# Kernel optimization log

Measured on AMD Instinct MI355X. Metric: run time of the kernel, lower is better.

## Reference

```python
import jax, jax.numpy as jnp
import numpy as np

D_MODEL = 512
D_FF = 2048
D_STATE = 16
D_CONV = 4
EXPAND = 2
D_INNER = EXPAND * D_MODEL
DT_RANK = (D_MODEL + 15) // 16  # 32
EPS = 1e-5


def silu(x):
    return x * jax.nn.sigmoid(x)


def layernorm(x, g, b):
    mu = jnp.mean(x, axis=-1, keepdims=True)
    var = jnp.mean(jnp.square(x - mu), axis=-1, keepdims=True)
    return (x - mu) * jax.lax.rsqrt(var + EPS) * g + b


def mamba_block(x, in_w, conv_w, conv_b, xproj_w, dt_w, dt_b, A_log, Dp, out_w):
    # x: (B, L, d_model)
    Bsz, L, _ = x.shape
    di = conv_w.shape[0]
    k = conv_w.shape[1]
    n = A_log.shape[1]
    r = dt_w.shape[1]
    xz = x @ in_w.T                      # (B, L, 2*di)
    xi, z = jnp.split(xz, 2, axis=-1)
    # causal depthwise conv1d
    xt = jnp.transpose(xi, (0, 2, 1))    # (B, di, L)
    xt = jnp.pad(xt, ((0, 0), (0, 0), (k - 1, 0)))
    xc = jax.lax.conv_general_dilated(
        xt, conv_w[:, None, :], (1,), 'VALID',
        feature_group_count=di,
        dimension_numbers=('NCH', 'OIH', 'NCH'))
    xc = silu(xc + conv_b[None, :, None])
    xc = jnp.transpose(xc, (0, 2, 1))    # (B, L, di)
    dbc = xc @ xproj_w.T                 # (B, L, r + 2n)
    dt = jax.nn.softplus(dbc[..., :r] @ dt_w.T + dt_b)   # (B, L, di)
    Bm = dbc[..., r:r + n]               # (B, L, n)
    Cm = dbc[..., r + n:]                # (B, L, n)
    A = -jnp.exp(A_log)                  # (di, n)

    def step(h, inp):
        dt_t, B_t, C_t, x_t = inp        # (B,di), (B,n), (B,n), (B,di)
        dA = jnp.exp(dt_t[..., None] * A)                 # (B, di, n)
        h = dA * h + (dt_t * x_t)[..., None] * B_t[:, None, :]
        y = jnp.einsum('bdn,bn->bd', h, C_t)
        return h, y

    xs = (jnp.moveaxis(dt, 1, 0), jnp.moveaxis(Bm, 1, 0),
          jnp.moveaxis(Cm, 1, 0), jnp.moveaxis(xc, 1, 0))
    h0 = jnp.zeros((Bsz, di, n), x.dtype)
    _, ys = jax.lax.scan(step, h0, xs)
    y = jnp.moveaxis(ys, 0, 1) + xc * Dp  # (B, L, di)
    y = y * silu(z)
    return y @ out_w.T                    # (B, L, d_model)


def setup_inputs() -> dict:
    key = jax.random.key(0)
    ks = iter(jax.random.split(key, 40))
    s = 0.02

    def mamba_params():
        return dict(
            in_w=jax.random.normal(next(ks), (2 * D_INNER, D_MODEL), jnp.float32) * s,
            conv_w=jax.random.normal(next(ks), (D_INNER, D_CONV), jnp.float32) * 0.3,
            conv_b=jnp.zeros((D_INNER,), jnp.float32),
            xproj_w=jax.random.normal(next(ks), (DT_RANK + 2 * D_STATE, D_INNER), jnp.float32) * s,
            dt_w=jax.random.normal(next(ks), (D_INNER, DT_RANK), jnp.float32) * 0.1,
            dt_b=jax.random.uniform(next(ks), (D_INNER,), jnp.float32, -4.0, -2.0),
            A_log=jnp.tile(jnp.log(jnp.arange(1, D_STATE + 1, dtype=jnp.float32)), (D_INNER, 1)),
            D=jnp.ones((D_INNER,), jnp.float32),
            out_w=jax.random.normal(next(ks), (D_MODEL, D_INNER), jnp.float32) * s,
        )

    pf = mamba_params()
    pb = mamba_params()
    inp = dict(
        x=jax.random.normal(next(ks), (8, 4096, D_MODEL), jnp.float32),
        f_in_w=pf['in_w'], f_conv_w=pf['conv_w'], f_conv_b=pf['conv_b'],
        f_xproj_w=pf['xproj_w'], f_dt_w=pf['dt_w'], f_dt_b=pf['dt_b'],
        f_A_log=pf['A_log'], f_D=pf['D'], f_out_w=pf['out_w'],
        b_in_w=pb['in_w'], b_conv_w=pb['conv_w'], b_conv_b=pb['conv_b'],
        b_xproj_w=pb['xproj_w'], b_dt_w=pb['dt_w'], b_dt_b=pb['dt_b'],
        b_A_log=pb['A_log'], b_D=pb['D'], b_out_w=pb['out_w'],
        ln_f_g=jnp.ones((D_MODEL,), jnp.float32), ln_f_b=jnp.zeros((D_MODEL,), jnp.float32),
        ln_b_g=jnp.ones((D_MODEL,), jnp.float32), ln_b_b=jnp.zeros((D_MODEL,), jnp.float32),
        ln_ff_g=jnp.ones((D_MODEL,), jnp.float32), ln_ff_b=jnp.zeros((D_MODEL,), jnp.float32),
        ffn_w1=jax.random.normal(next(ks), (D_FF, D_MODEL), jnp.float32) * s,
        ffn_b1=jnp.zeros((D_FF,), jnp.float32),
        ffn_w2=jax.random.normal(next(ks), (D_MODEL, D_FF), jnp.float32) * s,
        ffn_b2=jnp.zeros((D_MODEL,), jnp.float32),
    )
    return inp


def reference(x,
              f_in_w, f_conv_w, f_conv_b, f_xproj_w, f_dt_w, f_dt_b, f_A_log, f_D, f_out_w,
              b_in_w, b_conv_w, b_conv_b, b_xproj_w, b_dt_w, b_dt_b, b_A_log, b_D, b_out_w,
              ln_f_g, ln_f_b, ln_b_g, ln_b_b, ln_ff_g, ln_ff_b,
              ffn_w1, ffn_b1, ffn_w2, ffn_b2):
    # forward-direction mamba + AddNorm (dropout is identity at eval)
    mf = mamba_block(x, f_in_w, f_conv_w, f_conv_b, f_xproj_w, f_dt_w, f_dt_b,
                     f_A_log, f_D, f_out_w)
    out_f = layernorm(x + mf, ln_f_g, ln_f_b)
    # backward-direction: flip along seq, mamba, flip back
    mb = mamba_block(jnp.flip(x, axis=1), b_in_w, b_conv_w, b_conv_b, b_xproj_w,
                     b_dt_w, b_dt_b, b_A_log, b_D, b_out_w)
    out_b = jnp.flip(mb, axis=1)
    h = 0.5 * (out_f + layernorm(x + out_b, ln_b_g, ln_b_b))
    # FFN + AddNorm
    ff = jax.nn.gelu(h @ ffn_w1.T + ffn_b1) @ ffn_w2.T + ffn_b2
    return layernorm(h + ff, ln_ff_g, ln_ff_b)
```

## Files before the change

### kernel.cpp

```cpp
#include <hip/hip_runtime.h>
#include <hip/hip_bf16.h>
#include <math.h>


#define LSEQ 4096
#define DIN 1024
#define NST 16
#define CHUNK 64
#define NCHUNK 64
#define TCH 16

typedef __attribute__((ext_vector_type(8))) short bf16x8;
typedef __attribute__((ext_vector_type(4))) float f32x4;

typedef const __attribute__((address_space(1))) void* gas_ptr;
typedef __attribute__((address_space(3))) void* las_ptr;

__device__ __forceinline__ void load_lds16(const void* g, void* l) {
  __builtin_amdgcn_global_load_lds((gas_ptr)g, (las_ptr)l, 16, 0, 0);
}

__device__ __forceinline__ unsigned short bf16bits(float v) {
  __hip_bfloat16 h = __float2bfloat16(v);
  return *reinterpret_cast<unsigned short*>(&h);
}

__global__ void cast_bf16x4_kernel(const float4* __restrict__ src,
                                   ushort4* __restrict__ dst, int n4) {
  int i = blockIdx.x * 256 + threadIdx.x;
  if (i < n4) {
    float4 v = src[i];
    ushort4 o = {bf16bits(v.x), bf16bits(v.y), bf16bits(v.z), bf16bits(v.w)};
    dst[i] = o;
  }
}

__global__ void pad_xproj_kernel(const float* __restrict__ src,
                                 __hip_bfloat16* __restrict__ dst) {
  int i = blockIdx.x * 256 + threadIdx.x;
  int r = i >> 10, c = i & 1023;
  float v = (r < 64) ? src[r * 1024 + c] : 0.f;
  dst[i] = __float2bfloat16(v);
}

__global__ void zero4_kernel(float4* __restrict__ p, int n4) {
  int i = blockIdx.x * 256 + threadIdx.x;
  if (i < n4) p[i] = (float4){0.f, 0.f, 0.f, 0.f};
}

enum { EPI_BF16 = 0, EPI_F32 = 1, EPI_GELU_BF16 = 2, EPI_BIAS_BF16 = 3,
       EPI_F32_ATOM = 4, EPI_SPLIT_BF16 = 5 };

template <int EPI, int KSPLIT = 1>
__launch_bounds__(256)
__global__ void gemm_bt(const __hip_bfloat16* __restrict__ A,
                        const __hip_bfloat16* __restrict__ W,
                        void* __restrict__ Cout,
                        const float* __restrict__ bias,
                        void* __restrict__ Cout2,
                        int M, int N, int K) {
  __shared__ __align__(16) __hip_bfloat16 sA[128 * 64];
  __shared__ __align__(16) __hip_bfloat16 sB[128 * 64];
  const int tid  = threadIdx.x;
  const int wave = tid >> 6;
  const int lane = tid & 63;
  const int tileM = blockIdx.y * 128;
  const int tileN = blockIdx.x * 128;
  const int wrow = (wave >> 1) * 64;
  const int wcol = (wave & 1) * 64;

  f32x4 acc[4][4];
#pragma unroll
  for (int i = 0; i < 4; i++)
#pragma unroll
    for (int j = 0; j < 4; j++) acc[i][j] = (f32x4){0.f, 0.f, 0.f, 0.f};

  const int rbase = wave * 8 + (lane >> 3);
  const int segel = (((lane & 7) ^ (lane >> 3)) << 3);
  const int fr = lane & 15;
  const int fq = lane >> 4;

  const int kspan = K / KSPLIT;
  const int kbeg = (KSPLIT > 1) ? (int)blockIdx.z * kspan : 0;

  for (int k0 = kbeg; k0 < kbeg + kspan; k0 += 64) {
#pragma unroll
    for (int i = 0; i < 4; i++) {
      int r = i * 32 + rbase;
      const __hip_bfloat16* ga = A + (size_t)(tileM + r) * K + k0 + segel;
      const __hip_bfloat16* gb = W + (size_t)(tileN + r) * K + k0 + segel;
      int ldsoff = (i * 32 + wave * 8) * 64;
      load_lds16(ga, (void*)&sA[ldsoff]);
      load_lds16(gb, (void*)&sB[ldsoff]);
    }
    __syncthreads();
#pragma unroll
    for (int kt = 0; kt < 2; kt++) {
      bf16x8 af[4], bfm[4];
#pragma unroll
      for (int mt = 0; mt < 4; mt++) {
        int rm = wrow + mt * 16 + fr;
        int sg = (kt * 4 + fq) ^ (rm & 7);
        af[mt] = *(const bf16x8*)&sA[rm * 64 + sg * 8];
      }
#pragma unroll
      for (int nt = 0; nt < 4; nt++) {
        int rn = wcol + nt * 16 + fr;
        int sg = (kt * 4 + fq) ^ (rn & 7);
        bfm[nt] = *(const bf16x8*)&sB[rn * 64 + sg * 8];
      }
#pragma unroll
      for (int mt = 0; mt < 4; mt++)
#pragma unroll
        for (int nt = 0; nt < 4; nt++)
          acc[mt][nt] = __builtin_amdgcn_mfma_f32_16x16x32_bf16(
              af[mt], bfm[nt], acc[mt][nt], 0, 0, 0);
    }
    __syncthreads();
  }

#pragma unroll
  for (int mt = 0; mt < 4; mt++) {
#pragma unroll
    for (int nt = 0; nt < 4; nt++) {
      int col = tileN + wcol + nt * 16 + fr;
#pragma unroll
      for (int i = 0; i < 4; i++) {
        int row = tileM + wrow + mt * 16 + fq * 4 + i;
        float v = acc[mt][nt][i];
        size_t off = (size_t)row * N + col;
        if constexpr (EPI == EPI_BF16) {
          ((__hip_bfloat16*)Cout)[off] = __float2bfloat16(v);
        } else if constexpr (EPI == EPI_F32) {
          ((float*)Cout)[off] = v;
        } else if constexpr (EPI == EPI_F32_ATOM) {
          atomicAdd((float*)Cout + off, v);
        } else if constexpr (EPI == EPI_GELU_BF16) {
          float t = v + bias[col];
          float u0 = t + 0.044715f * t * t * t;
          float g = __fdividef(t, 1.f + __expf(-1.5957691216057308f * u0));
          ((__hip_bfloat16*)Cout)[off] = __float2bfloat16(g);
        } else if constexpr (EPI == EPI_BIAS_BF16) {
          ((__hip_bfloat16*)Cout)[off] = __float2bfloat16(v + bias[col]);
        } else {
          __hip_bfloat16* dst =
              (tileN < 1024) ? (__hip_bfloat16*)Cout : (__hip_bfloat16*)Cout2;
          int c2 = (tileN < 1024) ? col : (col - 1024);
          dst[(size_t)row * 1024 + c2] = __float2bfloat16(v);
        }
      }
    }
  }
}

__global__ void conv_silu_kernel(const __hip_bfloat16* __restrict__ xi,
                                 const float* __restrict__ cw,
                                 const float* __restrict__ cb,
                                 __hip_bfloat16* __restrict__ xc, int dir) {
  int row0 = blockIdx.x * TCH;
  int b = row0 >> 12, t0 = row0 & 4095;
  int d0 = threadIdx.x << 2;
  float w[4][4];
#pragma unroll
  for (int u = 0; u < 4; u++) {
    float4 wv = ((const float4*)cw)[d0 + u];
    w[u][0] = wv.x; w[u][1] = wv.y; w[u][2] = wv.z; w[u][3] = wv.w;
  }
  float4 bv = *(const float4*)(cb + d0);

  float win[3][4];
  auto loadrow = [&](int tau, float* o) {
    if (tau < 0) {
      o[0] = o[1] = o[2] = o[3] = 0.f;
    } else {
      int l = dir ? (LSEQ - 1 - tau) : tau;
      ushort4 v = *(const ushort4*)(xi + ((size_t)(b * LSEQ + l)) * DIN + d0);
      o[0] = __uint_as_float((unsigned)v.x << 16);
      o[1] = __uint_as_float((unsigned)v.y << 16);
      o[2] = __uint_as_float((unsigned)v.z << 16);
      o[3] = __uint_as_float((unsigned)v.w << 16);
    }
  };
  loadrow(t0 - 3, win[0]);
  loadrow(t0 - 2, win[1]);
  loadrow(t0 - 1, win[2]);

#pragma unroll
  for (int i = 0; i < TCH; i++) {
    int t = t0 + i;
    float cur[4];
    loadrow(t, cur);
    unsigned short o[4];
#pragma unroll
    for (int u = 0; u < 4; u++) {
      float s = (u == 0) ? bv.x : (u == 1) ? bv.y : (u == 2) ? bv.z : bv.w;
      s += w[u][0] * win[0][u] + w[u][1] * win[1][u] + w[u][2] * win[2][u] +
           w[u][3] * cur[u];
      float val = __fdividef(s, 1.f + __expf(-s));
      o[u] = bf16bits(val);
    }
    ushort4 o4 = {o[0], o[1], o[2], o[3]};
    *(ushort4*)(xc + (size_t)(row0 + i) * DIN + d0) = o4;
#pragma unroll
    for (int u = 0; u < 4; u++) {
      win[0][u] = win[1][u]; win[1][u] = win[2][u]; win[2][u] = cur[u];
    }
  }
}

__global__ void scan_pass1(const __hip_bfloat16* __restrict__ xc,
                           const float* __restrict__ dbc,
                           const float* __restrict__ dtw,
                           const float* __restrict__ dtbias,
                           __hip_bfloat16* __restrict__ dtb,
                           float* __restrict__ sumdt, float* __restrict__ hend) {
  __shared__ __align__(16) float sdbc[64 * 64];
  int d = blockIdx.x * 256 + threadIdx.x;
  int c = blockIdx.y, b = blockIdx.z;
  size_t rowbase = (size_t)b * LSEQ + (size_t)c * CHUNK;
  const float* gsrc = dbc + rowbase * 128;
#pragma unroll
  for (int v = 0; v < 4; v++) {
    int e = (v * 256 + threadIdx.x) * 4;
    int r = e >> 6, col = e & 63;
    *(float4*)&sdbc[e] = *(const float4*)&gsrc[(size_t)r * 128 + col];
  }
  __syncthreads();

  float w[32];
#pragma unroll
  for (int k = 0; k < 32; k++) w[k] = dtw[d * 32 + k];
  float bias = dtbias[d];
  float h[NST];
#pragma unroll
  for (int n = 0; n < NST; n++) h[n] = 0.f;
  float sd = 0.f;
  for (int i = 0; i < CHUNK; i++) {
    const float* rowp = &sdbc[i * 64];
    size_t row = rowbase + i;
    float a0 = bias, a1 = 0.f, a2 = 0.f, a3 = 0.f;
#pragma unroll
    for (int k = 0; k < 32; k += 4) {
      a0 += w[k] * rowp[k];
      a1 += w[k + 1] * rowp[k + 1];
      a2 += w[k + 2] * rowp[k + 2];
      a3 += w[k + 3] * rowp[k + 3];
    }
    float a = (a0 + a1) + (a2 + a3);
    float sp = (a > 20.f) ? a : __logf(1.f + __expf(a));
    __hip_bfloat16 dh = __float2bfloat16(sp);
    dtb[row * DIN + d] = dh;
    float dtv = __bfloat162float(dh);
    float xcv = __bfloat162float(xc[row * DIN + d]);
    float q = __expf(-dtv);
    float u0 = dtv * xcv;
    sd += dtv;
    float q2 = q * q, q3 = q2 * q, q4 = q2 * q2;
    float eg = 1.f;
#pragma unroll
    for (int g = 0; g < 4; g++) {
      float d1 = eg * q, d2 = eg * q2, d3 = eg * q3, d4 = eg * q4;
      h[4 * g + 0] = d1 * h[4 * g + 0] + u0 * rowp[32 + 4 * g + 0];
      h[4 * g + 1] = d2 * h[4 * g + 1] + u0 * rowp[32 + 4 * g + 1];
      h[4 * g + 2] = d3 * h[4 * g + 2] + u0 * rowp[32 + 4 * g + 2];
      h[4 * g + 3] = d4 * h[4 * g + 3] + u0 * rowp[32 + 4 * g + 3];
      eg = d4;
    }
  }
  sumdt[((size_t)b * NCHUNK + c) * DIN + d] = sd;
  size_t hb = (((size_t)b * NCHUNK + c) * NST) * DIN + d;
#pragma unroll
  for (int n = 0; n < NST; n++) hend[hb + (size_t)n * DIN] = h[n];
}

__global__ void scan_mid(const float* __restrict__ sumdt,
                         float* __restrict__ hh,
                         const float* __restrict__ A_log) {
  int d = blockIdx.x * 256 + threadIdx.x;
  int n = blockIdx.y, b = blockIdx.z;
  float An = -__expf(A_log[d * NST + n]);
  float h = 0.f;
  for (int c = 0; c < NCHUNK; c++) {
    size_t idx = (((size_t)b * NCHUNK + c) * NST + n) * DIN + d;
    float tmp = hh[idx];
    hh[idx] = h;
    float sd = sumdt[((size_t)b * NCHUNK + c) * DIN + d];
    h = __expf(An * sd) * h + tmp;
  }
}

__global__ void scan_pass3(__hip_bfloat16* xc_ym,
                           const __hip_bfloat16* __restrict__ dtb,
                           const float* __restrict__ dbc,
                           const float* __restrict__ hstart,
                           const __hip_bfloat16* __restrict__ z,
                           const float* __restrict__ Dp, int dir) {
  __shared__ __align__(16) float sdbc[64 * 64];
  int d = blockIdx.x * 256 + threadIdx.x;
  int c = blockIdx.y, b = blockIdx.z;
  size_t rowbase = (size_t)b * LSEQ + (size_t)c * CHUNK;
  const float* gsrc = dbc + rowbase * 128;
#pragma unroll
  for (int v = 0; v < 4; v++) {
    int e = (v * 256 + threadIdx.x) * 4;
    int r = e >> 6, col = e & 63;
    *(float4*)&sdbc[e] = *(const float4*)&gsrc[(size_t)r * 128 + col];
  }
  __syncthreads();

  float h[NST];
  size_t hb = (((size_t)b * NCHUNK + c) * NST) * DIN + d;
#pragma unroll
  for (int n = 0; n < NST; n++) h[n] = hstart[hb + (size_t)n * DIN];
  float Dd = Dp[d];
  for (int i = 0; i < CHUNK; i++) {
    const float* rowp = &sdbc[i * 64];
    size_t row = rowbase + i;
    int t = c * CHUNK + i;
    float dtv = __bfloat162float(dtb[row * DIN + d]);
    float xcv = __bfloat162float(xc_ym[row * DIN + d]);
    float q = __expf(-dtv);
    float u0 = dtv * xcv;
    float q2 = q * q, q3 = q2 * q, q4 = q2 * q2;
    float y0 = 0.f, y1 = 0.f, y2 = 0.f, y3 = 0.f;
    float eg = 1.f;
#pragma unroll
    for (int g = 0; g < 4; g++) {
      float d1 = eg * q, d2 = eg * q2, d3 = eg * q3, d4 = eg * q4;
      h[4 * g + 0] = d1 * h[4 * g + 0] + u0 * rowp[32 + 4 * g + 0];
      h[4 * g + 1] = d2 * h[4 * g + 1] + u0 * rowp[32 + 4 * g + 1];
      h[4 * g + 2] = d3 * h[4 * g + 2] + u0 * rowp[32 + 4 * g + 2];
      h[4 * g + 3] = d4 * h[4 * g + 3] + u0 * rowp[32 + 4 * g + 3];
      y0 += h[4 * g + 0] * rowp[48 + 4 * g + 0];
      y1 += h[4 * g + 1] * rowp[48 + 4 * g + 1];
      y2 += h[4 * g + 2] * rowp[48 + 4 * g + 2];
      y3 += h[4 * g + 3] * rowp[48 + 4 * g + 3];
      eg = d4;
    }
    float y = ((y0 + y1) + (y2 + y3)) + xcv * Dd;
    int zl = dir ? (LSEQ - 1 - t) : t;
    float zv = __bfloat162float(z[((size_t)(b * LSEQ + zl)) * DIN + d]);
    float gate = __fdividef(zv, 1.f + __expf(-zv));
    xc_ym[row * DIN + d] = __float2bfloat16(y * gate);
  }
}

__device__ __forceinline__ void block_reduce4(float4& v, float4* red) {
#pragma unroll
  for (int o = 32; o > 0; o >>= 1) {
    v.x += __shfl_down(v.x, o);
    v.y += __shfl_down(v.y, o);
    v.z += __shfl_down(v.z, o);
    v.w += __shfl_down(v.w, o);
  }
  int wave = threadIdx.x >> 6, lane = threadIdx.x & 63;
  if (lane == 0) red[wave] = v;
  __syncthreads();
  float4 a = red[0], b = red[1], c = red[2], d = red[3];
  v.x = a.x + b.x + c.x + d.x;
  v.y = a.y + b.y + c.y + d.y;
  v.z = a.z + b.z + c.z + d.z;
  v.w = a.w + b.w + c.w + d.w;
}

__global__ void ln_combine(const float* __restrict__ x,
                           const __hip_bfloat16* __restrict__ mf,
                           const __hip_bfloat16* __restrict__ mb,
                           const float* __restrict__ gf, const float* __restrict__ bf,
                           const float* __restrict__ gb, const float* __restrict__ bb,
                           __hip_bfloat16* __restrict__ h16) {
  __shared__ __align__(16) float4 red[4];
  int row = blockIdx.x;
  int b = row >> 12, l = row & 4095;
  const float* xr = x + (size_t)row * 512;
  const __hip_bfloat16* fr = mf + (size_t)row * 512;
  const __hip_bfloat16* br = mb + ((size_t)(b * LSEQ + (LSEQ - 1 - l))) * 512;
  int tid = threadIdx.x;
  float v1[2], v2[2];
  float4 s = {0.f, 0.f, 0.f, 0.f};
#pragma unroll
  for (int e = 0; e < 2; e++) {
    int i = tid + e * 256;
    float a = xr[i];
    v1[e] = a + __bfloat162float(fr[i]);
    v2[e] = a + __bfloat162float(br[i]);
    s.x += v1[e]; s.y += v1[e] * v1[e];
    s.z += v2[e]; s.w += v2[e] * v2[e];
  }
  block_reduce4(s, red);
  const float inv = 1.f / 512.f;
  float mu1 = s.x * inv, mu2 = s.z * inv;
  float r1 = rsqrtf(s.y * inv - mu1 * mu1 + 1e-5f);
  float r2 = rsqrtf(s.w * inv - mu2 * mu2 + 1e-5f);
#pragma unroll
  for (int e = 0; e < 2; e++) {
    int i = tid + e * 256;
    float of = (v1[e] - mu1) * r1 * gf[i] + bf[i];
    float ob = (v2[e] - mu2) * r2 * gb[i] + bb[i];
    h16[(size_t)row * 512 + i] = __float2bfloat16(0.5f * (of + ob));
  }
}

__global__ void ln_final(const __hip_bfloat16* __restrict__ h,
                         const __hip_bfloat16* __restrict__ f2,
                         const float* __restrict__ g, const float* __restrict__ bb,
                         float* __restrict__ out) {
  __shared__ __align__(16) float4 red[4];
  int row = blockIdx.x;
  int tid = threadIdx.x;
  float v[2];
  float4 s = {0.f, 0.f, 0.f, 0.f};
#pragma unroll
  for (int e = 0; e < 2; e++) {
    int i = tid + e * 256;
    v[e] = __bfloat162float(h[(size_t)row * 512 + i]) +
           __bfloat162float(f2[(size_t)row * 512 + i]);
    s.x += v[e]; s.y += v[e] * v[e];
  }
  block_reduce4(s, red);
  const float inv = 1.f / 512.f;
  float mu = s.x * inv;
  float r = rsqrtf(s.y * inv - mu * mu + 1e-5f);
#pragma unroll
  for (int e = 0; e < 2; e++) {
    int i = tid + e * 256;
    out[(size_t)row * 512 + i] = (v[e] - mu) * r * g[i] + bb[i];
  }
}

extern "C" void kernel_launch(void* const* d_in, const int* in_sizes, int n_in,
                              void* d_out, int out_size, void* d_ws, size_t ws_size,
                              hipStream_t stream) {
  const float* x = (const float*)d_in[0];
  const float* in_w[2]  = {(const float*)d_in[1],  (const float*)d_in[10]};
  const float* conv_w[2]= {(const float*)d_in[2],  (const float*)d_in[11]};
  const float* conv_b[2]= {(const float*)d_in[3],  (const float*)d_in[12]};
  const float* xproj[2] = {(const float*)d_in[4],  (const float*)d_in[13]};
  const float* dt_w[2]  = {(const float*)d_in[5],  (const float*)d_in[14]};
  const float* dt_b[2]  = {(const float*)d_in[6],  (const float*)d_in[15]};
  const float* A_log[2] = {(const float*)d_in[7],  (const float*)d_in[16]};
  const float* Dp[2]    = {(const float*)d_in[8],  (const float*)d_in[17]};
  const float* out_w[2] = {(const float*)d_in[9],  (const float*)d_in[18]};
  const float* ln_f_g = (const float*)d_in[19];
  const float* ln_f_b = (const float*)d_in[20];
  const float* ln_b_g = (const float*)d_in[21];
  const float* ln_b_b = (const float*)d_in[22];
  const float* ln_ff_g = (const float*)d_in[23];
  const float* ln_ff_b = (const float*)d_in[24];
  const float* ffn_w1 = (const float*)d_in[25];
  const float* ffn_b1 = (const float*)d_in[26];
  const float* ffn_w2 = (const float*)d_in[27];
  const float* ffn_b2 = (const float*)d_in[28];

  char* ws = (char*)d_ws;
  const size_t MiB = 1ull << 20;

  __hip_bfloat16* mdir[2] = {(__hip_bfloat16*)ws, (__hip_bfloat16*)(ws + 32 * MiB)};
  char* S = ws + 64 * MiB;

  __hip_bfloat16* xb = (__hip_bfloat16*)d_out;
  __hip_bfloat16* dtb = (__hip_bfloat16*)((char*)d_out + 32 * MiB);
  cast_bf16x4_kernel<<<16384, 256, 0, stream>>>((const float4*)x, (ushort4*)xb,
                                                4194304);

  int s = 8;
  if (ws_size >= 165 * MiB) s = 2;
  else if (ws_size >= 117 * MiB) s = 4;
  const int bb = 8 / s;
  const int Mc = bb * LSEQ;
  const size_t Cb = 64 * MiB / s;

  __hip_bfloat16* win  = (__hip_bfloat16*)S;
  __hip_bfloat16* wxp  = (__hip_bfloat16*)(S + 2 * MiB);
  __hip_bfloat16* wout = (__hip_bfloat16*)(S + 2 * MiB + 512 * 1024);
  char* BS = S + 4 * MiB;
  __hip_bfloat16* xi  = (__hip_bfloat16*)BS;
  __hip_bfloat16* zg  = (__hip_bfloat16*)(BS + Cb);
  __hip_bfloat16* xcd = (__hip_bfloat16*)(BS + 2 * Cb);
  float* dbc   = (float*)BS;
  float* sumdt = (float*)(BS + Cb / 4);
  float* hend  = (float*)(BS + Cb / 4 + Cb / 32);

  for (int dir = 0; dir < 2; dir++) {
    cast_bf16x4_kernel<<<1024, 256, 0, stream>>>((const float4*)in_w[dir],
                                                 (ushort4*)win, 262144);
    pad_xproj_kernel<<<512, 256, 0, stream>>>(xproj[dir], wxp);
    cast_bf16x4_kernel<<<512, 256, 0, stream>>>((const float4*)out_w[dir],
                                                (ushort4*)wout, 131072);
    for (int ci = 0; ci < s; ci++) {
      size_t m0 = (size_t)ci * Mc;
      gemm_bt<EPI_SPLIT_BF16><<<dim3(16, Mc / 128), 256, 0, stream>>>(
          xb + m0 * 512, win, xi, nullptr, zg, Mc, 2048, 512);
      conv_silu_kernel<<<Mc / TCH, 256, 0, stream>>>(xi, conv_w[dir],
                                                     conv_b[dir], xcd, dir);
      zero4_kernel<<<Mc / 8, 256, 0, stream>>>((float4*)dbc, Mc * 32);
      gemm_bt<EPI_F32_ATOM, 2><<<dim3(1, Mc / 128, 2), 256, 0, stream>>>(
          xcd, wxp, dbc, nullptr, nullptr, Mc, 128, 1024);
      scan_pass1<<<dim3(4, NCHUNK, bb), 256, 0, stream>>>(
          xcd, dbc, dt_w[dir], dt_b[dir], dtb, sumdt, hend);
      scan_mid<<<dim3(4, NST, bb), 256, 0, stream>>>(sumdt, hend, A_log[dir]);
      scan_pass3<<<dim3(4, NCHUNK, bb), 256, 0, stream>>>(
          xcd, dtb, dbc, hend, zg, Dp[dir], dir);
      gemm_bt<EPI_BF16><<<dim3(4, Mc / 128), 256, 0, stream>>>(
          xcd, wout, mdir[dir] + m0 * 512, nullptr, nullptr, Mc, 512, 1024);
    }
  }

  __hip_bfloat16* h16 = (__hip_bfloat16*)S;
  __hip_bfloat16* wf1 = (__hip_bfloat16*)(S + 32 * MiB);
  __hip_bfloat16* wf2 = (__hip_bfloat16*)(S + 34 * MiB);
  __hip_bfloat16* f2;
  __hip_bfloat16* g1 = (__hip_bfloat16*)ws;
  int sf;
  if (ws_size >= 132 * MiB) {
    f2 = (__hip_bfloat16*)(S + 36 * MiB);
    sf = 2;
  } else {
    f2 = (__hip_bfloat16*)(ws + 32 * MiB);
    sf = 4;
  }

  ln_combine<<<32768, 256, 0, stream>>>(x, mdir[0], mdir[1], ln_f_g, ln_f_b,
                                        ln_b_g, ln_b_b, h16);
  cast_bf16x4_kernel<<<1024, 256, 0, stream>>>((const float4*)ffn_w1,
                                               (ushort4*)wf1, 262144);
  cast_bf16x4_kernel<<<1024, 256, 0, stream>>>((const float4*)ffn_w2,
                                               (ushort4*)wf2, 262144);
  const int Mf = 32768 / sf;
  for (int ci = 0; ci < sf; ci++) {
    size_t m0 = (size_t)ci * Mf;
    gemm_bt<EPI_GELU_BF16><<<dim3(16, Mf / 128), 256, 0, stream>>>(
        h16 + m0 * 512, wf1, g1, ffn_b1, nullptr, Mf, 2048, 512);
    gemm_bt<EPI_BIAS_BF16><<<dim3(4, Mf / 128), 256, 0, stream>>>(
        g1, wf2, f2 + m0 * 512, ffn_b2, nullptr, Mf, 512, 2048);
  }
  ln_final<<<32768, 256, 0, stream>>>(h16, f2, ln_ff_g, ln_ff_b, (float*)d_out);
}
```

Measured before the change: 1.427 ms.

## Split scan state dimension across two half-waves per channel

Scan pass1 and pass3 now give each channel two lanes. Each lane handles 8 of the 16 state entries and half of the dt projection, and the partial sums are combined with a cross-lane shuffle. Twice as many blocks are launched, to raise parallelism and cut per-thread register pressure and serial latency in the scan loops. In exchange, every lane now does the exp and softplus work redundantly. Global stores are made by only half the lanes, and the xc/dt/z loads are duplicated across the two halves.

Result: slower. 1.673 ms (+17.2%).

```diff
diff --git a/kernel.cpp b/kernel.cpp
--- a/kernel.cpp
+++ b/kernel.cpp
@@ -215,62 +215,70 @@
                            __hip_bfloat16* __restrict__ dtb,
                            float* __restrict__ sumdt, float* __restrict__ hend) {
   __shared__ __align__(16) float sdbc[64 * 64];
-  int d = blockIdx.x * 256 + threadIdx.x;
-  int c = blockIdx.y, b = blockIdx.z;
+  const int tid = threadIdx.x;
+  const int wave = tid >> 6, lane = tid & 63;
+  const int ln = lane & 31, half = lane >> 5;
+  const int d = blockIdx.x * 128 + wave * 32 + ln;
+  const int c = blockIdx.y, b = blockIdx.z;
   size_t rowbase = (size_t)b * LSEQ + (size_t)c * CHUNK;
   const float* gsrc = dbc + rowbase * 128;
 #pragma unroll
   for (int v = 0; v < 4; v++) {
-    int e = (v * 256 + threadIdx.x) * 4;
+    int e = (v * 256 + tid) * 4;
     int r = e >> 6, col = e & 63;
     *(float4*)&sdbc[e] = *(const float4*)&gsrc[(size_t)r * 128 + col];
   }
   __syncthreads();
 
-  float w[32];
-#pragma unroll
-  for (int k = 0; k < 32; k++) w[k] = dtw[d * 32 + k];
-  float bias = dtbias[d];
-  float h[NST];
-#pragma unroll
-  for (int n = 0; n < NST; n++) h[n] = 0.f;
+  float w[16];
+#pragma unroll
+  for (int k = 0; k < 16; k++) w[k] = dtw[d * 32 + half * 16 + k];
+  const float bias = dtbias[d];
+  float h[8];
+#pragma unroll
+  for (int n = 0; n < 8; n++) h[n] = 0.f;
   float sd = 0.f;
   for (int i = 0; i < CHUNK; i++) {
     const float* rowp = &sdbc[i * 64];
     size_t row = rowbase + i;
-    float a0 = bias, a1 = 0.f, a2 = 0.f, a3 = 0.f;
-#pragma unroll
-    for (int k = 0; k < 32; k += 4) {
-      a0 += w[k] * rowp[k];
-      a1 += w[k + 1] * rowp[k + 1];
-      a2 += w[k + 2] * rowp[k + 2];
-      a3 += w[k + 3] * rowp[k + 3];
-    }
-    float a = (a0 + a1) + (a2 + a3);
+    float a0 = 0.f, a1 = 0.f, a2 = 0.f, a3 = 0.f;
+    const float* dp = rowp + half * 16;
+#pragma unroll
+    for (int k = 0; k < 16; k += 4) {
+      a0 += w[k] * dp[k];
+      a1 += w[k + 1] * dp[k + 1];
+      a2 += w[k + 2] * dp[k + 2];
+      a3 += w[k + 3] * dp[k + 3];
+    }
+    float ap = (a0 + a1) + (a2 + a3);
+    float a = ap + __shfl_xor(ap, 32) + bias;
     float sp = (a > 20.f) ? a : __logf(1.f + __expf(a));
     __hip_bfloat16 dh = __float2bfloat16(sp);
-    dtb[row * DIN + d] = dh;
+    if (half == 0) dtb[row * DIN + d] = dh;
     float dtv = __bfloat162float(dh);
     float xcv = __bfloat162float(xc[row * DIN + d]);
     float q = __expf(-dtv);
     float u0 = dtv * xcv;
     sd += dtv;
     float q2 = q * q, q3 = q2 * q, q4 = q2 * q2;
-    float eg = 1.f;
-#pragma unroll
-    for (int g = 0; g < 4; g++) {
+    float q8 = q4 * q4;
+    float eg = half ? q8 : 1.f;
+    const float* bp = rowp + 32 + half * 8;
+#pragma unroll
+    for (int g = 0; g < 2; g++) {
       float d1 = eg * q, d2 = eg * q2, d3 = eg * q3, d4 = eg * q4;
-      h[4 * g + 0] = d1 * h[4 * g + 0] + u0 * rowp[32 + 4 * g + 0];
-      h[4 * g + 1] = d2 * h[4 * g + 1] + u0 * rowp[32 + 4 * g + 1];
-      h[4 * g + 2] = d3 * h[4 * g + 2] + u0 * rowp[32 + 4 * g + 2];
-      h[4 * g + 3] = d4 * h[4 * g + 3] + u0 * rowp[32 + 4 * g + 3];
+      h[4 * g + 0] = d1 * h[4 * g + 0] + u0 * bp[4 * g + 0];
+      h[4 * g + 1] = d2 * h[4 * g + 1] + u0 * bp[4 * g + 1];
+      h[4 * g + 2] = d3 * h[4 * g + 2] + u0 * bp[4 * g + 2];
+      h[4 * g + 3] = d4 * h[4 * g + 3] + u0 * bp[4 * g + 3];
       eg = d4;
     }
   }
-  sumdt[((size_t)b * NCHUNK + c) * DIN + d] = sd;
+  if (half == 0) sumdt[((size_t)b * NCHUNK + c) * DIN + d] = sd;
   size_t hb = (((size_t)b * NCHUNK + c) * NST) * DIN + d;
 #pragma unroll
-  for (int n = 0; n < NST; n++) hend[hb + (size_t)n * DIN] = h[n];
+  for (int j = 0; j < 8; j++)
+    hend[hb + (size_t)(half * 8 + j) * DIN] = h[j];
 }
 
 __global__ void scan_mid(const float* __restrict__ sumdt,
@@ -296,23 +304,27 @@
                            const __hip_bfloat16* __restrict__ z,
                            const float* __restrict__ Dp, int dir) {
   __shared__ __align__(16) float sdbc[64 * 64];
-  int d = blockIdx.x * 256 + threadIdx.x;
-  int c = blockIdx.y, b = blockIdx.z;
+  const int tid = threadIdx.x;
+  const int wave = tid >> 6, lane = tid & 63;
+  const int ln = lane & 31, half = lane >> 5;
+  const int d = blockIdx.x * 128 + wave * 32 + ln;
+  const int c = blockIdx.y, b = blockIdx.z;
   size_t rowbase = (size_t)b * LSEQ + (size_t)c * CHUNK;
   const float* gsrc = dbc + rowbase * 128;
 #pragma unroll
   for (int v = 0; v < 4; v++) {
-    int e = (v * 256 + threadIdx.x) * 4;
+    int e = (v * 256 + tid) * 4;
     int r = e >> 6, col = e & 63;
     *(float4*)&sdbc[e] = *(const float4*)&gsrc[(size_t)r * 128 + col];
   }
   __syncthreads();
 
-  float h[NST];
+  float h[8];
   size_t hb = (((size_t)b * NCHUNK + c) * NST) * DIN + d;
 #pragma unroll
-  for (int n = 0; n < NST; n++) h[n] = hstart[hb + (size_t)n * DIN];
-  float Dd = Dp[d];
+  for (int j = 0; j < 8; j++)
+    h[j] = hstart[hb + (size_t)(half * 8 + j) * DIN];
+  const float Dd = Dp[d];
   for (int i = 0; i < CHUNK; i++) {
     const float* rowp = &sdbc[i * 64];
     size_t row = rowbase + i;
@@ -322,26 +334,33 @@
     float q = __expf(-dtv);
     float u0 = dtv * xcv;
     float q2 = q * q, q3 = q2 * q, q4 = q2 * q2;
+    float q8 = q4 * q4;
+    float eg = half ? q8 : 1.f;
     float y0 = 0.f, y1 = 0.f, y2 = 0.f, y3 = 0.f;
-    float eg = 1.f;
-#pragma unroll
-    for (int g = 0; g < 4; g++) {
+    const float* bp = rowp + 32 + half * 8;
+    const float* cp = rowp + 48 + half * 8;
+#pragma unroll
+    for (int g = 0; g < 2; g++) {
       float d1 = eg * q, d2 = eg * q2, d3 = eg * q3, d4 = eg * q4;
-      h[4 * g + 0] = d1 * h[4 * g + 0] + u0 * rowp[32 + 4 * g + 0];
-      h[4 * g + 1] = d2 * h[4 * g + 1] + u0 * rowp[32 + 4 * g + 1];
-      h[4 * g + 2] = d3 * h[4 * g + 2] + u0 * rowp[32 + 4 * g + 2];
-      h[4 * g + 3] = d4 * h[4 * g + 3] + u0 * rowp[32 + 4 * g + 3];
-      y0 += h[4 * g + 0] * rowp[48 + 4 * g + 0];
-      y1 += h[4 * g + 1] * rowp[48 + 4 * g + 1];
-      y2 += h[4 * g + 2] * rowp[48 + 4 * g + 2];
-      y3 += h[4 * g + 3] * rowp[48 + 4 * g + 3];
+      h[4 * g + 0] = d1 * h[4 * g + 0] + u0 * bp[4 * g + 0];
+      h[4 * g + 1] = d2 * h[4 * g + 1] + u0 * bp[4 * g + 1];
+      h[4 * g + 2] = d3 * h[4 * g + 2] + u0 * bp[4 * g + 2];
+      h[4 * g + 3] = d4 * h[4 * g + 3] + u0 * bp[4 * g + 3];
+      y0 += h[4 * g + 0] * cp[4 * g + 0];
+      y1 += h[4 * g + 1] * cp[4 * g + 1];
+      y2 += h[4 * g + 2] * cp[4 * g + 2];
+      y3 += h[4 * g + 3] * cp[4 * g + 3];
       eg = d4;
     }
-    float y = ((y0 + y1) + (y2 + y3)) + xcv * Dd;
-    int zl = dir ? (LSEQ - 1 - t) : t;
-    float zv = __bfloat162float(z[((size_t)(b * LSEQ + zl)) * DIN + d]);
-    float gate = __fdividef(zv, 1.f + __expf(-zv));
-    xc_ym[row * DIN + d] = __float2bfloat16(y * gate);
+    float yp = (y0 + y1) + (y2 + y3);
+    float y = yp + __shfl_xor(yp, 32);
+    if (half == 0) {
+      y += xcv * Dd;
+      int zl = dir ? (LSEQ - 1 - t) : t;
+      float zv = __bfloat162float(z[((size_t)(b * LSEQ + zl)) * DIN + d]);
+      float gate = __fdividef(zv, 1.f + __expf(-zv));
+      xc_ym[row * DIN + d] = __float2bfloat16(y * gate);
+    }
   }
 }
 
@@ -496,10 +515,10 @@
       zero4_kernel<<<Mc / 8, 256, 0, stream>>>((float4*)dbc, Mc * 32);
       gemm_bt<EPI_F32_ATOM, 2><<<dim3(1, Mc / 128, 2), 256, 0, stream>>>(
           xcd, wxp, dbc, nullptr, nullptr, Mc, 128, 1024);
-      scan_pass1<<<dim3(4, NCHUNK, bb), 256, 0, stream>>>(
+      scan_pass1<<<dim3(8, NCHUNK, bb), 256, 0, stream>>>(
           xcd, dbc, dt_w[dir], dt_b[dir], dtb, sumdt, hend);
       scan_mid<<<dim3(4, NST, bb), 256, 0, stream>>>(sumdt, hend, A_log[dir]);
-      scan_pass3<<<dim3(4, NCHUNK, bb), 256, 0, stream>>>(
+      scan_pass3<<<dim3(8, NCHUNK, bb), 256, 0, stream>>>(
           xcd, dtb, dbc, hend, zg, Dp[dir], dir);
       gemm_bt<EPI_BF16><<<dim3(4, Mc / 128), 256, 0, stream>>>(
           xcd, wout, mdir[dir] + m0 * 512, nullptr, nullptr, Mc, 512, 1024);
```

## Add 256x256-tile 8-wave pipelined GEMM for in-projection and FFN1

Applied to the files above, without the earlier changes.

Introduces a new bf16 MFMA GEMM kernel with 256x256 output tiles, 512 threads (8 waves), double-buffered LDS filled by direct global-to-LDS loads with XOR swizzle, and a staggered quarter-step schedule that overlaps loads with MFMA work across wave groups. It replaces the 128x128 GEMM for the in-projection (split epilogue) and the first FFN GEMM (GELU epilogue). The aim is more data reuse per loaded tile and better overlap of memory traffic with matrix math. In exchange it uses much more LDS and registers per block, which limits occupancy, and it relies on hand-placed waitcnt values being correct.

After: 1.498 ms. 5.0% more time.

```diff
diff --git a/kernel.cpp b/kernel.cpp
--- a/kernel.cpp
+++ b/kernel.cpp
@@ -50,6 +50,154 @@
 
 enum { EPI_BF16 = 0, EPI_F32 = 1, EPI_GELU_BF16 = 2, EPI_BIAS_BF16 = 3,
        EPI_F32_ATOM = 4, EPI_SPLIT_BF16 = 5 };
+
+template <int EPI>
+__launch_bounds__(512, 2)
+__global__ void gemm8(const __hip_bfloat16* __restrict__ A,
+                      const __hip_bfloat16* __restrict__ W,
+                      void* __restrict__ Cout,
+                      const float* __restrict__ bias,
+                      void* __restrict__ Cout2,
+                      int M, int N, int K) {
+  __shared__ __align__(16) __hip_bfloat16 sA[2 * 2 * 128 * 64];
+  __shared__ __align__(16) __hip_bfloat16 sB[2 * 2 * 128 * 64];
+  const int tid = threadIdx.x;
+  const int wid = tid >> 6;
+  const int lane = tid & 63;
+  const int fr = lane & 15, fq = lane >> 4;
+  const int wm = wid >> 2;
+  const int wn = wid & 3;
+  const int off = (wm == 0) ? (wn >> 1) : 2;
+  const int tileM = blockIdx.y * 256;
+  const int tileN = blockIdx.x * 256;
+  const int NT = K >> 6;
+  const int swz = fr & 7;
+
+  f32x4 acc[8][4];
+#pragma unroll
+  for (int i = 0; i < 8; i++)
+#pragma unroll
+    for (int j = 0; j < 4; j++) acc[i][j] = (f32x4){0.f, 0.f, 0.f, 0.f};
+
+  bf16x8 af[4][2];
+  bf16x8 bf0[2][2];
+  bf16x8 bf1[2][2];
+
+  auto stage = [&](int t, int k) {
+    const int half = (k == 0) ? 0 : (k == 3) ? 1 : (k - 1);
+    const bool isA = (k == 0 || k == 3);
+    const int buf = t & 1;
+    const __hip_bfloat16* mat = isA ? A : W;
+    const int mbase = isA ? tileM : tileN;
+    __hip_bfloat16* lds = isA ? sA : sB;
+#pragma unroll
+    for (int r = 0; r < 2; r++) {
+      int rh = r * 64 + wid * 8 + (lane >> 3);
+      int kseg = (lane & 7) ^ (lane >> 3);
+      const __hip_bfloat16* src =
+          mat + (size_t)(mbase + half * 128 + rh) * K + t * 64 + kseg * 8;
+      load_lds16(src,
+                 (void*)&lds[((buf * 2 + half) * 128 + r * 64 + wid * 8) * 64]);
+    }
+  };
+
+#define READ_A(buf, mh)                                                       \
+  {                                                                           \
+    const __hip_bfloat16* base_ = &sA[(((buf)*2 + wm) * 128 + (mh)*64) * 64]; \
+    _Pragma("unroll") for (int mt = 0; mt < 4; mt++)                          \
+        _Pragma("unroll") for (int kk = 0; kk < 2; kk++) {                    \
+      int slot = (kk * 4 + fq) ^ swz;                                         \
+      af[mt][kk] = *(const bf16x8*)&base_[(mt * 16 + fr) * 64 + slot * 8];    \
+    }                                                                         \
+  }
+#define READ_B(buf, nh, arr)                                                  \
+  {                                                                           \
+    const __hip_bfloat16* base_ =                                             \
+        &sB[(((buf)*2 + (wn >> 1)) * 128 + (wn & 1) * 64 + (nh)*32) * 64];    \
+    _Pragma("unroll") for (int nt = 0; nt < 2; nt++)                          \
+        _Pragma("unroll") for (int kk = 0; kk < 2; kk++) {                    \
+      int slot = (kk * 4 + fq) ^ swz;                                         \
+      arr[nt][kk] = *(const bf16x8*)&base_[(nt * 16 + fr) * 64 + slot * 8];   \
+    }                                                                         \
+  }
+#define MFMA_Q(mh, nh, arr)                                                   \
+  {                                                                           \
+    _Pragma("unroll") for (int mt = 0; mt < 4; mt++)                          \
+        _Pragma("unroll") for (int nt = 0; nt < 2; nt++)                      \
+            _Pragma("unroll") for (int kk = 0; kk < 2; kk++)                  \
+                acc[(mh)*4 + mt][(nh)*2 + nt] =                               \
+        __builtin_amdgcn_mfma_f32_16x16x32_bf16(                              \
+            af[mt][kk], arr[nt][kk], acc[(mh)*4 + mt][(nh)*2 + nt], 0, 0, 0); \
+  }
+
+  stage(0, 0); stage(0, 1); stage(0, 2); stage(0, 3);
+
+  const int GP = 4 * NT + 2;
+  for (int g = 0; g < GP; g++) {
+    const int tcur = g >> 2, k = g & 3;
+    if (tcur < NT) {
+      if (tcur == NT - 1) {
+        if (k == 0) asm volatile("s_waitcnt vmcnt(4)" ::: "memory");
+        else if (k == 1) asm volatile("s_waitcnt vmcnt(2)" ::: "memory");
+        else if (k == 2) asm volatile("s_waitcnt vmcnt(0)" ::: "memory");
+      } else {
+        if (k < 3) asm volatile("s_waitcnt vmcnt(4)" ::: "memory");
+      }
+    }
+    __builtin_amdgcn_s_barrier();
+    __builtin_amdgcn_sched_barrier(0);
+    const int gg = g - off;
+    const bool valid = (gg >= 0) && ((gg >> 2) < NT);
+    const int tw = gg >> 2, q = gg & 3;
+    const int buf = tw & 1;
+    if (valid) {
+      if (q == 0)      { READ_A(buf, 0); READ_B(buf, 0, bf0); }
+      else if (q == 1) { READ_B(buf, 1, bf1); }
+      else if (q == 2) { READ_A(buf, 1); }
+    }
+    if (tcur + 1 < NT) stage(tcur + 1, k);
+    if (valid) {
+      __builtin_amdgcn_s_setprio(1);
+      if (q == 0)      MFMA_Q(0, 0, bf0)
+      else if (q == 1) MFMA_Q(0, 1, bf1)
+      else if (q == 2) MFMA_Q(1, 1, bf1)
+      else             MFMA_Q(1, 0, bf0)
+      __builtin_amdgcn_s_setprio(0);
+    }
+  }
+
+#pragma unroll
+  for (int mt = 0; mt < 8; mt++) {
+#pragma unroll
+    for (int nt = 0; nt < 4; nt++) {
+      int col = tileN + wn * 64 + nt * 16 + fr;
+#pragma unroll
+      for (int i = 0; i < 4; i++) {
+        int row = tileM + wm * 128 + mt * 16 + fq * 4 + i;
+        float v = acc[mt][nt][i];
+        size_t offst = (size_t)row * N + col;
+        if constexpr (EPI == EPI_BF16) {
+          ((__hip_bfloat16*)Cout)[offst] = __float2bfloat16(v);
+        } else if constexpr (EPI == EPI_GELU_BF16) {
+          float t = v + bias[col];
+          float u0 = t + 0.044715f * t * t * t;
+          float gl = __fdividef(t, 1.f + __expf(-1.5957691216057308f * u0));
+          ((__hip_bfloat16*)Cout)[offst] = __float2bfloat16(gl);
+        } else if constexpr (EPI == EPI_BIAS_BF16) {
+          ((__hip_bfloat16*)Cout)[offst] = __float2bfloat16(v + bias[col]);
+        } else {
+          __hip_bfloat16* dst =
+              (tileN < 1024) ? (__hip_bfloat16*)Cout : (__hip_bfloat16*)Cout2;
+          int c2 = (tileN < 1024) ? col : (col - 1024);
+          dst[(size_t)row * 1024 + c2] = __float2bfloat16(v);
+        }
+      }
+    }
+  }
+#undef READ_A
+#undef READ_B
+#undef MFMA_Q
+}
 
 template <int EPI, int KSPLIT = 1>
 __launch_bounds__(256)
@@ -489,7 +637,7 @@
                                                 (ushort4*)wout, 131072);
     for (int ci = 0; ci < s; ci++) {
       size_t m0 = (size_t)ci * Mc;
-      gemm_bt<EPI_SPLIT_BF16><<<dim3(16, Mc / 128), 256, 0, stream>>>(
+      gemm8<EPI_SPLIT_BF16><<<dim3(8, Mc / 256), 512, 0, stream>>>(
           xb + m0 * 512, win, xi, nullptr, zg, Mc, 2048, 512);
       conv_silu_kernel<<<Mc / TCH, 256, 0, stream>>>(xi, conv_w[dir],
                                                      conv_b[dir], xcd, dir);
@@ -529,7 +677,7 @@
   const int Mf = 32768 / sf;
   for (int ci = 0; ci < sf; ci++) {
     size_t m0 = (size_t)ci * Mf;
-    gemm_bt<EPI_GELU_BF16><<<dim3(16, Mf / 128), 256, 0, stream>>>(
+    gemm8<EPI_GELU_BF16><<<dim3(8, Mf / 256), 512, 0, stream>>>(
         h16 + m0 * 512, wf1, g1, ffn_b1, nullptr, Mf, 2048, 512);
     gemm_bt<EPI_BIAS_BF16><<<dim3(4, Mf / 128), 256, 0, stream>>>(
         g1, wf2, f2 + m0 * 512, ffn_b2, nullptr, Mf, 512, 2048);
```
